# Kernel optimization log

Measured on AMD Instinct MI355X. Metric: run time of the kernel, lower is better.

## Reference

```python
import jax, jax.numpy as jnp
import numpy as np

N_NODES = 100000
N_EDGES = 1600000
D_IN = 64
D_OUT = 64
BN_EPS = 1e-5


def setup_inputs() -> dict:
    key = jax.random.key(0)
    k_x, k_src, k_dst, k_ew, k_w = jax.random.split(key, 5)
    x = jax.random.normal(k_x, (N_NODES, D_IN), dtype=jnp.float32)
    edge_src = jax.random.randint(k_src, (N_EDGES,), 0, N_NODES, dtype=jnp.int32)
    edge_dst = jax.random.randint(k_dst, (N_EDGES,), 0, N_NODES, dtype=jnp.int32)
    edge_weight = jax.random.uniform(k_ew, (N_EDGES,), dtype=jnp.float32)
    # Xavier-uniform weight, zero bias (reset_parameters)
    limit = float(np.sqrt(6.0 / (D_IN + D_OUT)))
    W = jax.random.uniform(k_w, (D_IN, D_OUT), dtype=jnp.float32, minval=-limit, maxval=limit)
    bias = jnp.zeros((D_OUT,), dtype=jnp.float32)
    gamma = jnp.ones((D_OUT,), dtype=jnp.float32)
    beta = jnp.zeros((D_OUT,), dtype=jnp.float32)
    return {"x": x, "edge_src": edge_src, "edge_dst": edge_dst,
            "edge_weight": edge_weight, "W": W, "bias": bias,
            "gamma": gamma, "beta": beta}


def reference(x, edge_src, edge_dst, edge_weight, W, bias, gamma, beta):
    # GraphConvolution: support = x @ W  -> [N, D_OUT]
    support = jnp.matmul(x, W)
    # spmm(adj, support) with adj in COO form: out[d] += w_e * support[s]
    msgs = edge_weight[:, None] * support[edge_src]        # [E, D_OUT]
    agg = jax.ops.segment_sum(msgs, edge_dst, num_segments=N_NODES)
    out = agg + bias
    # BatchNorm1d (training mode: batch statistics over node dim)
    mean = jnp.mean(out, axis=0)
    var = jnp.var(out, axis=0)
    out = (out - mean) * jax.lax.rsqrt(var + BN_EPS) * gamma + beta
    # ReLU activation; dropout is identity in deterministic/inference mode
    return jax.nn.relu(out)
```

## Files before the change

kernel.cpp:

```cpp
#include <hip/hip_runtime.h>
#include <hip/hip_bf16.h>

#define NN 100000
#define NE 1600000
#define DD 64
#define NCOARSE 98
#define GEMM_TILES 1563
#define PLACE_EPB 2048
#define PLACE_BLOCKS 782
#define LCNT_STRIDE 800
#define STAT_BLOCKS 256

__device__ inline unsigned short f2bf(float f) {
    __hip_bfloat16 h = __float2bfloat16(f);
    unsigned short s; __builtin_memcpy(&s, &h, 2); return s;
}
__device__ inline float pw(unsigned p) { return __uint_as_float((p & 0xFFFE0000u) >> 1); }

__global__ __launch_bounds__(256) void k_gemm_hist(const float* __restrict__ x,
                                                   const float* __restrict__ Wg,
                                                   unsigned* __restrict__ support2,
                                                   const int* __restrict__ edst,
                                                   int* __restrict__ lcntT) {
    if (blockIdx.x >= GEMM_TILES) {
        __shared__ int h[NCOARSE];
        const int blk = blockIdx.x - GEMM_TILES;
        for (int i = threadIdx.x; i < NCOARSE; i += 256) h[i] = 0;
        __syncthreads();
        const int e0 = blk * PLACE_EPB;
#pragma unroll
        for (int k = 0; k < 8; ++k) {
            int e = e0 + k * 256 + threadIdx.x;
            if (e < NE) atomicAdd(&h[edst[e] >> 10], 1);
        }
        __syncthreads();
        for (int i = threadIdx.x; i < NCOARSE; i += 256)
            lcntT[i * LCNT_STRIDE + blk] = h[i];
        return;
    }

    __shared__ float Ws[DD * DD];
    __shared__ float Xs[64 * DD];
    const int r0 = blockIdx.x * 64;
    const int nrows = (r0 + 64 <= NN) ? 64 : (NN - r0);

    for (int i = threadIdx.x; i < DD * DD / 4; i += 256)
        ((float4*)Ws)[i] = ((const float4*)Wg)[i];
    const float4* xg = (const float4*)(x + (size_t)r0 * DD);
    for (int i = threadIdx.x; i < nrows * 16; i += 256)
        ((float4*)Xs)[i] = xg[i];
    __syncthreads();

    const int wave = threadIdx.x >> 6, lane = threadIdx.x & 63;
    const int half = lane >> 5, hl = lane & 31;
    const int rbase = wave * 16 + half * 8;

    float acc0[8] = {0.f, 0.f, 0.f, 0.f, 0.f, 0.f, 0.f, 0.f};
    float acc1[8] = {0.f, 0.f, 0.f, 0.f, 0.f, 0.f, 0.f, 0.f};
#pragma unroll 4
    for (int k = 0; k < DD; k += 4) {
        float2 w0 = *(const float2*)&Ws[(k + 0) * DD + 2 * hl];
        float2 w1 = *(const float2*)&Ws[(k + 1) * DD + 2 * hl];
        float2 w2 = *(const float2*)&Ws[(k + 2) * DD + 2 * hl];
        float2 w3 = *(const float2*)&Ws[(k + 3) * DD + 2 * hl];
#pragma unroll
        for (int r = 0; r < 8; ++r) {
            float4 xv = *(const float4*)&Xs[(rbase + r) * DD + k];
            acc0[r] = fmaf(xv.x, w0.x, acc0[r]); acc1[r] = fmaf(xv.x, w0.y, acc1[r]);
            acc0[r] = fmaf(xv.y, w1.x, acc0[r]); acc1[r] = fmaf(xv.y, w1.y, acc1[r]);
            acc0[r] = fmaf(xv.z, w2.x, acc0[r]); acc1[r] = fmaf(xv.z, w2.y, acc1[r]);
            acc0[r] = fmaf(xv.w, w3.x, acc0[r]); acc1[r] = fmaf(xv.w, w3.y, acc1[r]);
        }
    }
#pragma unroll
    for (int r = 0; r < 8; ++r) {
        const int row = rbase + r;
        if (row < nrows) {
            unsigned p = (unsigned)f2bf(acc0[r]) | ((unsigned)f2bf(acc1[r]) << 16);
            support2[(size_t)(r0 + row) * 32 + hl] = p;
        }
    }
}

__global__ __launch_bounds__(256) void k_colscan(int* __restrict__ lcntT,
                                                 int* __restrict__ cnt98) {
    int* col = lcntT + blockIdx.x * LCNT_STRIDE;
    const int t = threadIdx.x, base = t * 4;
    int v[4], s = 0;
#pragma unroll
    for (int j = 0; j < 4; ++j) {
        v[j] = (base + j < PLACE_BLOCKS) ? col[base + j] : 0;
        s += v[j];
    }
    __shared__ int sc[256];
    sc[t] = s; __syncthreads();
    for (int o = 1; o < 256; o <<= 1) {
        int u = (t >= o) ? sc[t - o] : 0;
        __syncthreads();
        sc[t] += u;
        __syncthreads();
    }
    int run = sc[t] - s;
#pragma unroll
    for (int j = 0; j < 4; ++j) {
        if (base + j < PLACE_BLOCKS) col[base + j] = run;
        run += v[j];
    }
    if (t == 255) cnt98[blockIdx.x] = sc[255];
}

__global__ __launch_bounds__(128) void k_scan98(const int* __restrict__ cnt98,
                                                int* __restrict__ cstart,
                                                int* __restrict__ bstart) {
    __shared__ int sc[128];
    const int t = threadIdx.x;
    const int v = (t < NCOARSE) ? cnt98[t] : 0;
    sc[t] = v; __syncthreads();
    for (int o = 1; o < 128; o <<= 1) {
        int u = (t >= o) ? sc[t - o] : 0;
        __syncthreads();
        sc[t] += u;
        __syncthreads();
    }
    if (t < NCOARSE) cstart[t] = sc[t] - v;
    if (t == 0) { cstart[NCOARSE] = NE; bstart[NN] = NE; }
}

__global__ __launch_bounds__(256) void k_pa_scatter(const int* __restrict__ esrc,
                                                    const int* __restrict__ edst,
                                                    const float* __restrict__ ew,
                                                    const int* __restrict__ cstart,
                                                    const int* __restrict__ lcntT,
                                                    int2* __restrict__ permA) {
    __shared__ int loff[NCOARSE];
    for (int i = threadIdx.x; i < NCOARSE; i += 256)
        loff[i] = cstart[i] + lcntT[i * LCNT_STRIDE + blockIdx.x];
    __syncthreads();
    const int e0 = blockIdx.x * PLACE_EPB;
#pragma unroll
    for (int k = 0; k < 8; ++k) {
        int e = e0 + k * 256 + threadIdx.x;
        if (e < NE) {
            int d = edst[e];
            int p = atomicAdd(&loff[d >> 10], 1);
            permA[p] = make_int2(esrc[e] | ((d & 1023) << 20), __float_as_int(ew[e]));
        }
    }
}

__global__ __launch_bounds__(1024) void k_placeB(const int* __restrict__ cstart,
                                                 const int2* __restrict__ permA,
                                                 unsigned* __restrict__ perm,
                                                 int* __restrict__ bstart) {
    __shared__ int sc[1024], loff[1024], wtot[16];
    const int c = blockIdx.x, t = threadIdx.x;
    const int wave = t >> 6, lane = t & 63;
    const int cs = cstart[c], ce = cstart[c + 1];
    sc[t] = 0;
    __syncthreads();
    for (int j = cs + t; j < ce; j += 1024)
        atomicAdd(&sc[(permA[j].x >> 20) & 1023], 1);
    __syncthreads();
    const int v = sc[t];
    int xv = v;
#pragma unroll
    for (int o = 1; o < 64; o <<= 1) {
        int u = __shfl_up(xv, o, 64);
        if (lane >= o) xv += u;
    }
    if (lane == 63) wtot[wave] = xv;
    __syncthreads();
    if (t < 16) {
        int w = wtot[t];
        int xw = w;
#pragma unroll
        for (int o = 1; o < 16; o <<= 1) {
            int u = __shfl_up(xw, o, 64);
            if (t >= o) xw += u;
        }
        wtot[t] = xw - w;
    }
    __syncthreads();
    const int base = cs + wtot[wave] + xv - v;
    loff[t] = base;
    const int node = c * 1024 + t;
    if (node < NN) bstart[node] = base;
    __syncthreads();
    for (int j = cs + t; j < ce; j += 1024) {
        int2 m = permA[j];
        int p = atomicAdd(&loff[(m.x >> 20) & 1023], 1);
        unsigned wb = (unsigned)(f2bf(__int_as_float(m.y)) & 0x7FFF);
        perm[p] = (unsigned)(m.x & 0x1FFFF) | (wb << 17);
    }
}

__global__ __launch_bounds__(256) void k_gather(const int* __restrict__ bstart,
                                                const unsigned* __restrict__ perm,
                                                const unsigned* __restrict__ support2,
                                                float* __restrict__ out) {
    const int wave = threadIdx.x >> 6, lane = threadIdx.x & 63;
    const int half = lane >> 5, hl = lane & 31;
    const int d = blockIdx.x * 4 + wave;
    const int bs = bstart[d], be = bstart[d + 1];
    float accx[4] = {0.f, 0.f, 0.f, 0.f};
    float accy[4] = {0.f, 0.f, 0.f, 0.f};
    int j0 = bs;
    for (; j0 + 15 < be; j0 += 16) {
        unsigned m[8], p[8];
#pragma unroll
        for (int i = 0; i < 8; ++i) m[i] = perm[j0 + 2 * i + half];
#pragma unroll
        for (int i = 0; i < 8; ++i) p[i] = support2[(size_t)(m[i] & 0x1FFFF) * 32 + hl];
#pragma unroll
        for (int i = 0; i < 8; ++i) {
            float w = pw(m[i]);
            accx[i & 3] = fmaf(w, __uint_as_float(p[i] << 16), accx[i & 3]);
            accy[i & 3] = fmaf(w, __uint_as_float(p[i] & 0xffff0000u), accy[i & 3]);
        }
    }
    for (; j0 + 7 < be; j0 += 8) {
        unsigned m[4], p[4];
#pragma unroll
        for (int i = 0; i < 4; ++i) m[i] = perm[j0 + 2 * i + half];
#pragma unroll
        for (int i = 0; i < 4; ++i) p[i] = support2[(size_t)(m[i] & 0x1FFFF) * 32 + hl];
#pragma unroll
        for (int i = 0; i < 4; ++i) {
            float w = pw(m[i]);
            accx[i] = fmaf(w, __uint_as_float(p[i] << 16), accx[i]);
            accy[i] = fmaf(w, __uint_as_float(p[i] & 0xffff0000u), accy[i]);
        }
    }
    for (; j0 + 3 < be; j0 += 4) {
        unsigned m0 = perm[j0 + half];
        unsigned m1 = perm[j0 + 2 + half];
        unsigned p0 = support2[(size_t)(m0 & 0x1FFFF) * 32 + hl];
        unsigned p1 = support2[(size_t)(m1 & 0x1FFFF) * 32 + hl];
        float w0 = pw(m0), w1 = pw(m1);
        accx[0] = fmaf(w0, __uint_as_float(p0 << 16), accx[0]);
        accy[0] = fmaf(w0, __uint_as_float(p0 & 0xffff0000u), accy[0]);
        accx[1] = fmaf(w1, __uint_as_float(p1 << 16), accx[1]);
        accy[1] = fmaf(w1, __uint_as_float(p1 & 0xffff0000u), accy[1]);
    }
    for (; j0 + half < be; j0 += 2) {
        unsigned m = perm[j0 + half];
        unsigned p = support2[(size_t)(m & 0x1FFFF) * 32 + hl];
        float w = pw(m);
        accx[0] = fmaf(w, __uint_as_float(p << 16), accx[0]);
        accy[0] = fmaf(w, __uint_as_float(p & 0xffff0000u), accy[0]);
    }
    float ax = (accx[0] + accx[1]) + (accx[2] + accx[3]);
    float ay = (accy[0] + accy[1]) + (accy[2] + accy[3]);
    ax += __shfl_xor(ax, 32);
    ay += __shfl_xor(ay, 32);
    if (half == 0)
        *(float2*)(out + (size_t)d * DD + 2 * hl) = make_float2(ax, ay);
}

__device__ inline float4 shfl_down4(float4 v, int dd) {
    v.x = __shfl_down(v.x, dd, 64); v.y = __shfl_down(v.y, dd, 64);
    v.z = __shfl_down(v.z, dd, 64); v.w = __shfl_down(v.w, dd, 64);
    return v;
}
__device__ inline float4 add4(float4 a, float4 b) {
    a.x += b.x; a.y += b.y; a.z += b.z; a.w += b.w; return a;
}

__global__ __launch_bounds__(256) void k_stats(const float* __restrict__ agg,
                                               float* __restrict__ pstat) {
    const int lane = threadIdx.x & 63, wave = threadIdx.x >> 6;
    const int q = lane & 15, sub = lane >> 4;
    float4 s = {0, 0, 0, 0}, sq = {0, 0, 0, 0};
    const int stride = gridDim.x * 16;
    for (int row = (blockIdx.x * 4 + wave) * 4 + sub; row < NN; row += stride) {
        float4 v = *(const float4*)(agg + (size_t)row * DD + q * 4);
        s.x += v.x; s.y += v.y; s.z += v.z; s.w += v.w;
        sq.x = fmaf(v.x, v.x, sq.x); sq.y = fmaf(v.y, v.y, sq.y);
        sq.z = fmaf(v.z, v.z, sq.z); sq.w = fmaf(v.w, v.w, sq.w);
    }
    s = add4(s, shfl_down4(s, 32));  s = add4(s, shfl_down4(s, 16));
    sq = add4(sq, shfl_down4(sq, 32)); sq = add4(sq, shfl_down4(sq, 16));

    __shared__ float red[2][4][DD];
    if (lane < 16) {
        red[0][wave][q * 4 + 0] = s.x;  red[0][wave][q * 4 + 1] = s.y;
        red[0][wave][q * 4 + 2] = s.z;  red[0][wave][q * 4 + 3] = s.w;
        red[1][wave][q * 4 + 0] = sq.x; red[1][wave][q * 4 + 1] = sq.y;
        red[1][wave][q * 4 + 2] = sq.z; red[1][wave][q * 4 + 3] = sq.w;
    }
    __syncthreads();
    if (threadIdx.x < 2 * DD) {
        const int t = threadIdx.x;
        const int part = t >> 6, c = t & 63;
        pstat[blockIdx.x * 2 * DD + t] =
            red[part][0][c] + red[part][1][c] + red[part][2][c] + red[part][3][c];
    }
}

__global__ __launch_bounds__(128) void k_finstats(const float* __restrict__ pstat,
                                                  float* __restrict__ ss,
                                                  const float* __restrict__ gamma,
                                                  const float* __restrict__ beta) {
    const int t = threadIdx.x;
    float acc = 0.f;
    for (int b = 0; b < STAT_BLOCKS; ++b)
        acc += pstat[b * 2 * DD + t];
    __shared__ float red[2 * DD];
    red[t] = acc;
    __syncthreads();
    if (t < DD) {
        const float invn = 1.0f / NN;
        float mean = red[t] * invn;
        float var = fmaxf(red[DD + t] * invn - mean * mean, 0.f);
        float sc = rsqrtf(var + 1e-5f) * gamma[t];
        ss[t] = sc;
        ss[DD + t] = beta[t] - mean * sc;
    }
}

__global__ __launch_bounds__(256) void k_final(float* __restrict__ out,
                                               const float* __restrict__ ss) {
    const size_t idx = ((size_t)blockIdx.x * 256 + threadIdx.x) * 4;
    const int c = (int)(idx & 63);
    float4 v = *(const float4*)(out + idx);
    float4 o;
    o.x = fmaxf(fmaf(v.x, ss[c + 0], ss[DD + c + 0]), 0.f);
    o.y = fmaxf(fmaf(v.y, ss[c + 1], ss[DD + c + 1]), 0.f);
    o.z = fmaxf(fmaf(v.z, ss[c + 2], ss[DD + c + 2]), 0.f);
    o.w = fmaxf(fmaf(v.w, ss[c + 3], ss[DD + c + 3]), 0.f);
    *(float4*)(out + idx) = o;
}

extern "C" void kernel_launch(void* const* d_in, const int* in_sizes, int n_in,
                              void* d_out, int out_size, void* d_ws, size_t ws_size,
                              hipStream_t stream) {
    const float* x     = (const float*)d_in[0];
    const int*   esrc  = (const int*)d_in[1];
    const int*   edst  = (const int*)d_in[2];
    const float* ew    = (const float*)d_in[3];
    const float* W     = (const float*)d_in[4];
    const float* gamma = (const float*)d_in[6];
    const float* beta  = (const float*)d_in[7];
    float*       out   = (float*)d_out;

    char* ws = (char*)d_ws;
    unsigned* support2 = (unsigned*)ws;  ws += (size_t)NN * DD * 2;
    int2*     permA  = (int2*)ws;     ws += (size_t)NE * 8;
    unsigned* perm   = (unsigned*)ws; ws += (size_t)NE * 4;
    int*   lcntT  = (int*)ws;    ws += NCOARSE * LCNT_STRIDE * 4;
    int*   cnt98  = (int*)ws;    ws += NCOARSE * 4;
    float* ss     = (float*)ws;  ws += 128 * 4;
    int*   cstart = (int*)ws;    ws += (NCOARSE + 1) * 4;
    int*   bstart = (int*)ws;    ws += (NN + 4) * 4;
    float* pstat  = (float*)ws;  ws += STAT_BLOCKS * 2 * DD * 4;


    k_gemm_hist <<<GEMM_TILES + PLACE_BLOCKS, 256, 0, stream>>>(x, W, support2, edst, lcntT);
    k_colscan   <<<NCOARSE, 256, 0, stream>>>(lcntT, cnt98);
    k_scan98    <<<1, 128, 0, stream>>>(cnt98, cstart, bstart);
    k_pa_scatter<<<PLACE_BLOCKS, 256, 0, stream>>>(esrc, edst, ew, cstart, lcntT, permA);
    k_placeB    <<<NCOARSE, 1024, 0, stream>>>(cstart, permA, perm, bstart);
    k_gather    <<<NN / 4, 256, 0, stream>>>(bstart, perm, support2, out);
    k_stats     <<<STAT_BLOCKS, 256, 0, stream>>>(out, pstat);
    k_finstats  <<<1, 128, 0, stream>>>(pstat, ss, gamma, beta);
    k_final     <<<NN * DD / 4 / 256, 256, 0, stream>>>(out, ss);
}
```

Before: 219.8 us.

## Double coarse buckets and gather support rows with 16-byte lane loads

After: 217.3 us. About the same (-1.1%).

```diff
diff --git a/kernel.cpp b/kernel.cpp
--- a/kernel.cpp
+++ b/kernel.cpp
@@ -4,7 +4,7 @@
 #define NN 100000
 #define NE 1600000
 #define DD 64
-#define NCOARSE 98
+#define NCOARSE 196
 #define GEMM_TILES 1563
 #define PLACE_EPB 2048
 #define PLACE_BLOCKS 782
@@ -31,7 +31,7 @@
 #pragma unroll
         for (int k = 0; k < 8; ++k) {
             int e = e0 + k * 256 + threadIdx.x;
-            if (e < NE) atomicAdd(&h[edst[e] >> 10], 1);
+            if (e < NE) atomicAdd(&h[edst[e] >> 9], 1);
         }
         __syncthreads();
         for (int i = threadIdx.x; i < NCOARSE; i += 256)
@@ -83,7 +83,7 @@
 }
 
 __global__ __launch_bounds__(256) void k_colscan(int* __restrict__ lcntT,
-                                                 int* __restrict__ cnt98) {
+                                                 int* __restrict__ cnt) {
     int* col = lcntT + blockIdx.x * LCNT_STRIDE;
     const int t = threadIdx.x, base = t * 4;
     int v[4], s = 0;
@@ -106,17 +106,17 @@
         if (base + j < PLACE_BLOCKS) col[base + j] = run;
         run += v[j];
     }
-    if (t == 255) cnt98[blockIdx.x] = sc[255];
-}
-
-__global__ __launch_bounds__(128) void k_scan98(const int* __restrict__ cnt98,
-                                                int* __restrict__ cstart,
-                                                int* __restrict__ bstart) {
-    __shared__ int sc[128];
+    if (t == 255) cnt[blockIdx.x] = sc[255];
+}
+
+__global__ __launch_bounds__(256) void k_scan196(const int* __restrict__ cnt,
+                                                 int* __restrict__ cstart,
+                                                 int* __restrict__ bstart) {
+    __shared__ int sc[256];
     const int t = threadIdx.x;
-    const int v = (t < NCOARSE) ? cnt98[t] : 0;
+    const int v = (t < NCOARSE) ? cnt[t] : 0;
     sc[t] = v; __syncthreads();
-    for (int o = 1; o < 128; o <<= 1) {
+    for (int o = 1; o < 256; o <<= 1) {
         int u = (t >= o) ? sc[t - o] : 0;
         __syncthreads();
         sc[t] += u;
@@ -142,8 +142,8 @@
         int e = e0 + k * 256 + threadIdx.x;
         if (e < NE) {
             int d = edst[e];
-            int p = atomicAdd(&loff[d >> 10], 1);
-            permA[p] = make_int2(esrc[e] | ((d & 1023) << 20), __float_as_int(ew[e]));
+            int p = atomicAdd(&loff[d >> 9], 1);
+            permA[p] = make_int2(esrc[e] | ((d & 511) << 17), __float_as_int(ew[e]));
         }
     }
 }
@@ -152,43 +152,47 @@
                                                  const int2* __restrict__ permA,
                                                  unsigned* __restrict__ perm,
                                                  int* __restrict__ bstart) {
-    __shared__ int sc[1024], loff[1024], wtot[16];
+    __shared__ int sc[512], loff[512], wtot[8];
     const int c = blockIdx.x, t = threadIdx.x;
     const int wave = t >> 6, lane = t & 63;
     const int cs = cstart[c], ce = cstart[c + 1];
-    sc[t] = 0;
+    if (t < 512) sc[t] = 0;
     __syncthreads();
     for (int j = cs + t; j < ce; j += 1024)
-        atomicAdd(&sc[(permA[j].x >> 20) & 1023], 1);
-    __syncthreads();
-    const int v = sc[t];
-    int xv = v;
-#pragma unroll
-    for (int o = 1; o < 64; o <<= 1) {
-        int u = __shfl_up(xv, o, 64);
-        if (lane >= o) xv += u;
-    }
-    if (lane == 63) wtot[wave] = xv;
-    __syncthreads();
-    if (t < 16) {
-        int w = wtot[t];
-        int xw = w;
-#pragma unroll
-        for (int o = 1; o < 16; o <<= 1) {
+        atomicAdd(&sc[(permA[j].x >> 17) & 511], 1);
+    __syncthreads();
+    int v = 0, xv = 0;
+    if (wave < 8) {
+        v = sc[t];
+        xv = v;
+#pragma unroll
+        for (int o = 1; o < 64; o <<= 1) {
+            int u = __shfl_up(xv, o, 64);
+            if (lane >= o) xv += u;
+        }
+        if (lane == 63) wtot[wave] = xv;
+    }
+    __syncthreads();
+    if (t < 8) {
+        int w = wtot[t], xw = w;
+#pragma unroll
+        for (int o = 1; o < 8; o <<= 1) {
             int u = __shfl_up(xw, o, 64);
             if (t >= o) xw += u;
         }
         wtot[t] = xw - w;
     }
     __syncthreads();
-    const int base = cs + wtot[wave] + xv - v;
-    loff[t] = base;
-    const int node = c * 1024 + t;
-    if (node < NN) bstart[node] = base;
+    if (wave < 8) {
+        const int base = cs + wtot[wave] + xv - v;
+        loff[t] = base;
+        const int node = c * 512 + t;
+        if (node < NN) bstart[node] = base;
+    }
     __syncthreads();
     for (int j = cs + t; j < ce; j += 1024) {
         int2 m = permA[j];
-        int p = atomicAdd(&loff[(m.x >> 20) & 1023], 1);
+        int p = atomicAdd(&loff[(m.x >> 17) & 511], 1);
         unsigned wb = (unsigned)(f2bf(__int_as_float(m.y)) & 0x7FFF);
         perm[p] = (unsigned)(m.x & 0x1FFFF) | (wb << 17);
     }
@@ -196,65 +200,63 @@
 
 __global__ __launch_bounds__(256) void k_gather(const int* __restrict__ bstart,
                                                 const unsigned* __restrict__ perm,
-                                                const unsigned* __restrict__ support2,
+                                                const uint4* __restrict__ support4,
                                                 float* __restrict__ out) {
     const int wave = threadIdx.x >> 6, lane = threadIdx.x & 63;
-    const int half = lane >> 5, hl = lane & 31;
+    const int sub = lane >> 3, q = lane & 7;
     const int d = blockIdx.x * 4 + wave;
     const int bs = bstart[d], be = bstart[d + 1];
-    float accx[4] = {0.f, 0.f, 0.f, 0.f};
-    float accy[4] = {0.f, 0.f, 0.f, 0.f};
+    float acc[8] = {0.f, 0.f, 0.f, 0.f, 0.f, 0.f, 0.f, 0.f};
     int j0 = bs;
     for (; j0 + 15 < be; j0 += 16) {
-        unsigned m[8], p[8];
-#pragma unroll
-        for (int i = 0; i < 8; ++i) m[i] = perm[j0 + 2 * i + half];
-#pragma unroll
-        for (int i = 0; i < 8; ++i) p[i] = support2[(size_t)(m[i] & 0x1FFFF) * 32 + hl];
-#pragma unroll
-        for (int i = 0; i < 8; ++i) {
-            float w = pw(m[i]);
-            accx[i & 3] = fmaf(w, __uint_as_float(p[i] << 16), accx[i & 3]);
-            accy[i & 3] = fmaf(w, __uint_as_float(p[i] & 0xffff0000u), accy[i & 3]);
-        }
-    }
-    for (; j0 + 7 < be; j0 += 8) {
-        unsigned m[4], p[4];
-#pragma unroll
-        for (int i = 0; i < 4; ++i) m[i] = perm[j0 + 2 * i + half];
-#pragma unroll
-        for (int i = 0; i < 4; ++i) p[i] = support2[(size_t)(m[i] & 0x1FFFF) * 32 + hl];
-#pragma unroll
-        for (int i = 0; i < 4; ++i) {
-            float w = pw(m[i]);
-            accx[i] = fmaf(w, __uint_as_float(p[i] << 16), accx[i]);
-            accy[i] = fmaf(w, __uint_as_float(p[i] & 0xffff0000u), accy[i]);
-        }
-    }
-    for (; j0 + 3 < be; j0 += 4) {
-        unsigned m0 = perm[j0 + half];
-        unsigned m1 = perm[j0 + 2 + half];
-        unsigned p0 = support2[(size_t)(m0 & 0x1FFFF) * 32 + hl];
-        unsigned p1 = support2[(size_t)(m1 & 0x1FFFF) * 32 + hl];
-        float w0 = pw(m0), w1 = pw(m1);
-        accx[0] = fmaf(w0, __uint_as_float(p0 << 16), accx[0]);
-        accy[0] = fmaf(w0, __uint_as_float(p0 & 0xffff0000u), accy[0]);
-        accx[1] = fmaf(w1, __uint_as_float(p1 << 16), accx[1]);
-        accy[1] = fmaf(w1, __uint_as_float(p1 & 0xffff0000u), accy[1]);
-    }
-    for (; j0 + half < be; j0 += 2) {
-        unsigned m = perm[j0 + half];
-        unsigned p = support2[(size_t)(m & 0x1FFFF) * 32 + hl];
-        float w = pw(m);
-        accx[0] = fmaf(w, __uint_as_float(p << 16), accx[0]);
-        accy[0] = fmaf(w, __uint_as_float(p & 0xffff0000u), accy[0]);
-    }
-    float ax = (accx[0] + accx[1]) + (accx[2] + accx[3]);
-    float ay = (accy[0] + accy[1]) + (accy[2] + accy[3]);
-    ax += __shfl_xor(ax, 32);
-    ay += __shfl_xor(ay, 32);
-    if (half == 0)
-        *(float2*)(out + (size_t)d * DD + 2 * hl) = make_float2(ax, ay);
+        unsigned mA = perm[j0 + sub];
+        unsigned mB = perm[j0 + 8 + sub];
+        uint4 pA = support4[(size_t)(mA & 0x1FFFF) * 8 + q];
+        uint4 pB = support4[(size_t)(mB & 0x1FFFF) * 8 + q];
+        float wA = pw(mA), wB = pw(mB);
+        acc[0] = fmaf(wA, __uint_as_float(pA.x << 16), acc[0]);
+        acc[1] = fmaf(wA, __uint_as_float(pA.x & 0xffff0000u), acc[1]);
+        acc[2] = fmaf(wA, __uint_as_float(pA.y << 16), acc[2]);
+        acc[3] = fmaf(wA, __uint_as_float(pA.y & 0xffff0000u), acc[3]);
+        acc[4] = fmaf(wA, __uint_as_float(pA.z << 16), acc[4]);
+        acc[5] = fmaf(wA, __uint_as_float(pA.z & 0xffff0000u), acc[5]);
+        acc[6] = fmaf(wA, __uint_as_float(pA.w << 16), acc[6]);
+        acc[7] = fmaf(wA, __uint_as_float(pA.w & 0xffff0000u), acc[7]);
+        acc[0] = fmaf(wB, __uint_as_float(pB.x << 16), acc[0]);
+        acc[1] = fmaf(wB, __uint_as_float(pB.x & 0xffff0000u), acc[1]);
+        acc[2] = fmaf(wB, __uint_as_float(pB.y << 16), acc[2]);
+        acc[3] = fmaf(wB, __uint_as_float(pB.y & 0xffff0000u), acc[3]);
+        acc[4] = fmaf(wB, __uint_as_float(pB.z << 16), acc[4]);
+        acc[5] = fmaf(wB, __uint_as_float(pB.z & 0xffff0000u), acc[5]);
+        acc[6] = fmaf(wB, __uint_as_float(pB.w << 16), acc[6]);
+        acc[7] = fmaf(wB, __uint_as_float(pB.w & 0xffff0000u), acc[7]);
+    }
+    for (; j0 < be; j0 += 8) {
+        if (j0 + sub < be) {
+            unsigned m = perm[j0 + sub];
+            uint4 p = support4[(size_t)(m & 0x1FFFF) * 8 + q];
+            float w = pw(m);
+            acc[0] = fmaf(w, __uint_as_float(p.x << 16), acc[0]);
+            acc[1] = fmaf(w, __uint_as_float(p.x & 0xffff0000u), acc[1]);
+            acc[2] = fmaf(w, __uint_as_float(p.y << 16), acc[2]);
+            acc[3] = fmaf(w, __uint_as_float(p.y & 0xffff0000u), acc[3]);
+            acc[4] = fmaf(w, __uint_as_float(p.z << 16), acc[4]);
+            acc[5] = fmaf(w, __uint_as_float(p.z & 0xffff0000u), acc[5]);
+            acc[6] = fmaf(w, __uint_as_float(p.w << 16), acc[6]);
+            acc[7] = fmaf(w, __uint_as_float(p.w & 0xffff0000u), acc[7]);
+        }
+    }
+#pragma unroll
+    for (int i = 0; i < 8; ++i) {
+        acc[i] += __shfl_xor(acc[i], 8, 64);
+        acc[i] += __shfl_xor(acc[i], 16, 64);
+        acc[i] += __shfl_xor(acc[i], 32, 64);
+    }
+    if (sub == 0) {
+        float* op = out + (size_t)d * DD + q * 8;
+        *(float4*)op = make_float4(acc[0], acc[1], acc[2], acc[3]);
+        *(float4*)(op + 4) = make_float4(acc[4], acc[5], acc[6], acc[7]);
+    }
 }
 
 __device__ inline float4 shfl_down4(float4 v, int dd) {
@@ -348,7 +350,7 @@
     int2*     permA  = (int2*)ws;     ws += (size_t)NE * 8;
     unsigned* perm   = (unsigned*)ws; ws += (size_t)NE * 4;
     int*   lcntT  = (int*)ws;    ws += NCOARSE * LCNT_STRIDE * 4;
-    int*   cnt98  = (int*)ws;    ws += NCOARSE * 4;
+    int*   cnt    = (int*)ws;    ws += NCOARSE * 4;
     float* ss     = (float*)ws;  ws += 128 * 4;
     int*   cstart = (int*)ws;    ws += (NCOARSE + 1) * 4;
     int*   bstart = (int*)ws;    ws += (NN + 4) * 4;
@@ -356,11 +358,11 @@
 
 
     k_gemm_hist <<<GEMM_TILES + PLACE_BLOCKS, 256, 0, stream>>>(x, W, support2, edst, lcntT);
-    k_colscan   <<<NCOARSE, 256, 0, stream>>>(lcntT, cnt98);
-    k_scan98    <<<1, 128, 0, stream>>>(cnt98, cstart, bstart);
+    k_colscan   <<<NCOARSE, 256, 0, stream>>>(lcntT, cnt);
+    k_scan196   <<<1, 256, 0, stream>>>(cnt, cstart, bstart);
     k_pa_scatter<<<PLACE_BLOCKS, 256, 0, stream>>>(esrc, edst, ew, cstart, lcntT, permA);
     k_placeB    <<<NCOARSE, 1024, 0, stream>>>(cstart, permA, perm, bstart);
-    k_gather    <<<NN / 4, 256, 0, stream>>>(bstart, perm, support2, out);
+    k_gather    <<<NN / 4, 256, 0, stream>>>(bstart, perm, (const uint4*)support2, out);
     k_stats     <<<STAT_BLOCKS, 256, 0, stream>>>(out, pstat);
     k_finstats  <<<1, 128, 0, stream>>>(pstat, ss, gamma, beta);
     k_final     <<<NN * DD / 4 / 256, 256, 0, stream>>>(out, ss);
```
